# Kernel optimization log

Measured on AMD Instinct MI355X. Metric: run time of the kernel, lower is better.

## Reference

```python
import jax, jax.numpy as jnp
import numpy as np

N_NODES = 100000
N_EDGES = 1600000
NFEAT, NHID, NCLASS = 256, 512, 256


def _init_params(key):
    ks = jax.random.split(key, 8)
    s = 0.02
    p = {
        'W1a': jax.random.normal(ks[0], (NFEAT, NHID), jnp.float32) * s,
        'b1a': jnp.zeros((NHID,), jnp.float32),
        'W1b': jax.random.normal(ks[1], (NHID, NHID), jnp.float32) * s,
        'b1b': jnp.zeros((NHID,), jnp.float32),
        'W2a': jax.random.normal(ks[2], (NHID, NHID), jnp.float32) * s,
        'b2a': jnp.zeros((NHID,), jnp.float32),
        'W2b': jax.random.normal(ks[3], (NHID, NCLASS), jnp.float32) * s,
        'b2b': jnp.zeros((NCLASS,), jnp.float32),
        'eps1': jnp.zeros((), jnp.float32),
        'eps2': jnp.zeros((), jnp.float32),
    }
    return p


def setup_inputs() -> dict:
    key = jax.random.key(0)
    kx, ke, kp = jax.random.split(key, 3)
    x = jax.random.normal(kx, (N_NODES, NFEAT), jnp.float32)
    edge_index = jax.random.randint(ke, (2, N_EDGES), 0, N_NODES, jnp.int64)
    inp = {'x': x, 'edge_index': edge_index}
    inp.update(_init_params(kp))
    return inp


def _gin_agg(h, src, dst, eps, n_nodes):
    # sum of neighbor (source) features at each destination node + (1+eps)*self
    agg = jax.ops.segment_sum(h[src], dst, num_segments=n_nodes)
    return (1.0 + eps) * h + agg


def reference(x, edge_index, W1a, b1a, W1b, b1b, W2a, b2a, W2b, b2b, eps1, eps2):
    src, dst = edge_index[0], edge_index[1]
    n = x.shape[0]
    # GINConv layer 1: MLP = Linear-ReLU-Linear-ReLU
    h = _gin_agg(x, src, dst, eps1, n)
    h = jax.nn.relu(h @ W1a + b1a)
    h = jax.nn.relu(h @ W1b + b1b)
    # dropout: eval mode (identity)
    # GINConv layer 2: MLP = Linear-ReLU-Linear
    h = _gin_agg(h, src, dst, eps2, n)
    h = jax.nn.relu(h @ W2a + b2a)
    out = h @ W2b + b2b
    return out
```

## Files before the change

kernel.cpp:

```cpp
#include <hip/hip_runtime.h>
#include <hip/hip_bf16.h>
#include <stdint.h>

#define NN 100000
#define NFEATD 256
#define NHIDD 512
#define NCLASSD 256

typedef short bf16x8 __attribute__((ext_vector_type(8)));
typedef float f32x4 __attribute__((ext_vector_type(4)));
typedef float f32x2 __attribute__((ext_vector_type(2)));

__device__ __forceinline__ float bf2f(uint32_t u) {
    union { uint32_t i; float f; } v; v.i = u << 16; return v.f;
}
__device__ __forceinline__ ushort f2bf(float f) {
    uint32_t x = __float_as_uint(f);
    uint32_t r = (x + 0x7FFF + ((x >> 16) & 1)) >> 16;
    return (ushort)r;
}

__global__ void zero_i32(int* __restrict__ p, int n) {
    int i = blockIdx.x * 256 + threadIdx.x;
    if (i < n) p[i] = 0;
}

__global__ void count_deg(const int* __restrict__ dst, int* __restrict__ deg, int nE) {
    int e = blockIdx.x * 256 + threadIdx.x;
    if (e < nE) atomicAdd(&deg[dst[e]], 1);
}

__global__ __launch_bounds__(1024) void scan_excl(const int* __restrict__ deg,
                                                  int* __restrict__ off, int n) {
    __shared__ int wsum[16];
    __shared__ int carry_s;
    const int tid = threadIdx.x;
    const int lane = tid & 63, wv = tid >> 6;
    if (tid == 0) carry_s = 0;
    __syncthreads();
    for (int base = 0; base < n; base += 1024) {
        int i = base + tid;
        int v = (i < n) ? deg[i] : 0;
        int x = v;
#pragma unroll
        for (int d = 1; d < 64; d <<= 1) {
            int y = __shfl_up(x, d, 64);
            if (lane >= d) x += y;
        }
        if (lane == 63) wsum[wv] = x;
        __syncthreads();
        if (wv == 0 && lane < 16) {
            int s = wsum[lane];
#pragma unroll
            for (int d = 1; d < 16; d <<= 1) {
                int y = __shfl_up(s, d, 16);
                if (lane >= d) s += y;
            }
            wsum[lane] = s;
        }
        __syncthreads();
        int carry = carry_s;
        int wprefix = (wv == 0) ? 0 : wsum[wv - 1];
        if (i < n) off[i] = carry + wprefix + x - v;
        __syncthreads();
        if (tid == 0) carry_s = carry + wsum[15];
        __syncthreads();
    }
    if (tid == 0) off[n] = carry_s;
}

__global__ void fill_csr(const int* __restrict__ src, const int* __restrict__ dst,
                         const int* __restrict__ off, int* __restrict__ cursor,
                         int* __restrict__ csr, int nE) {
    int e = blockIdx.x * 256 + threadIdx.x;
    if (e >= nE) return;
    int d = dst[e];
    int p = off[d] + atomicAdd(&cursor[d], 1);
    csr[p] = src[e];
}

__global__ void prep_w4(const float* __restrict__ W1a, const float* __restrict__ W1b,
                        const float* __restrict__ W2a, const float* __restrict__ W2b,
                        ushort* __restrict__ Wt1a, ushort* __restrict__ Wt1b,
                        ushort* __restrict__ Wt2a, ushort* __restrict__ Wt2b) {
    int idx = blockIdx.x * 256 + threadIdx.x;
    if (idx < 131072) {
        int k = idx >> 9, n = idx & 511;
        Wt1a[n * 256 + k] = f2bf(W1a[idx]);
    } else if (idx < 131072 + 262144) {
        int i = idx - 131072;
        int k = i >> 9, n = i & 511;
        Wt1b[n * 512 + k] = f2bf(W1b[i]);
    } else if (idx < 131072 + 524288) {
        int i = idx - (131072 + 262144);
        int k = i >> 9, n = i & 511;
        Wt2a[n * 512 + k] = f2bf(W2a[i]);
    } else if (idx < 131072 + 524288 + 131072) {
        int i = idx - (131072 + 524288);
        int k = i >> 8, n = i & 255;
        Wt2b[n * 512 + k] = f2bf(W2b[i]);
    }
}

__global__ void cast_f32_fp8(const float* __restrict__ a, uint8_t* __restrict__ o, int n) {
    int i = (blockIdx.x * 256 + threadIdx.x) * 8;
    if (i >= n) return;
    float4 v0 = *(const float4*)(a + i);
    float4 v1 = *(const float4*)(a + i + 4);
    int lo = __builtin_amdgcn_cvt_pk_fp8_f32(v0.x, v0.y, 0, false);
    lo = __builtin_amdgcn_cvt_pk_fp8_f32(v0.z, v0.w, lo, true);
    int hi = __builtin_amdgcn_cvt_pk_fp8_f32(v1.x, v1.y, 0, false);
    hi = __builtin_amdgcn_cvt_pk_fp8_f32(v1.z, v1.w, hi, true);
    uint2 r; r.x = (uint32_t)lo; r.y = (uint32_t)hi;
    *(uint2*)(o + i) = r;
}

__device__ __forceinline__ void accp(uint32_t p, f32x2& lo, f32x2& hi) {
    lo += __builtin_amdgcn_cvt_pk_f32_fp8((int)p, false);
    hi += __builtin_amdgcn_cvt_pk_f32_fp8((int)p, true);
}

__global__ void gather256f8(const uint8_t* __restrict__ X8, const int* __restrict__ off,
                            const int* __restrict__ csr, const float* __restrict__ eps,
                            ushort* __restrict__ out) {
    int node = (blockIdx.x * 256 + threadIdx.x) >> 6;
    if (node >= NN) return;
    int lane = threadIdx.x & 63;
    float sc = 1.0f + *eps;
    f32x2 scv = {sc, sc};
    const uint32_t* X1 = (const uint32_t*)X8;
    f32x2 lo = {0.f, 0.f}, hi = {0.f, 0.f};
    {
        uint32_t p = X1[(size_t)node * 64 + lane];
        lo = scv * __builtin_amdgcn_cvt_pk_f32_fp8((int)p, false);
        hi = scv * __builtin_amdgcn_cvt_pk_f32_fp8((int)p, true);
    }
    int e = off[node], e1 = off[node + 1];
    for (; e + 7 < e1; e += 8) {
        uint32_t p[8];
#pragma unroll
        for (int t = 0; t < 8; ++t) p[t] = X1[(size_t)csr[e + t] * 64 + lane];
#pragma unroll
        for (int t = 0; t < 8; ++t) accp(p[t], lo, hi);
    }
    for (; e < e1; ++e)
        accp(X1[(size_t)csr[e] * 64 + lane], lo, hi);
    uint2 r;
    r.x = (uint32_t)f2bf(lo[0]) | ((uint32_t)f2bf(lo[1]) << 16);
    r.y = (uint32_t)f2bf(hi[0]) | ((uint32_t)f2bf(hi[1]) << 16);
    *(uint2*)(out + (size_t)node * 256 + lane * 4) = r;
}

__global__ void gather512f8(const uint8_t* __restrict__ H8, const int* __restrict__ off,
                            const int* __restrict__ csr, const float* __restrict__ eps,
                            ushort* __restrict__ out) {
    int node = (blockIdx.x * 256 + threadIdx.x) >> 6;
    if (node >= NN) return;
    int lane = threadIdx.x & 63;
    float sc = 1.0f + *eps;
    f32x2 scv = {sc, sc};
    const uint2* H2 = (const uint2*)H8;
    f32x2 l0 = {0.f, 0.f}, h0 = {0.f, 0.f}, l1 = {0.f, 0.f}, h1 = {0.f, 0.f};
    {
        uint2 p = H2[(size_t)node * 64 + lane];
        l0 = scv * __builtin_amdgcn_cvt_pk_f32_fp8((int)p.x, false);
        h0 = scv * __builtin_amdgcn_cvt_pk_f32_fp8((int)p.x, true);
        l1 = scv * __builtin_amdgcn_cvt_pk_f32_fp8((int)p.y, false);
        h1 = scv * __builtin_amdgcn_cvt_pk_f32_fp8((int)p.y, true);
    }
    int e = off[node], e1 = off[node + 1];
    for (; e + 7 < e1; e += 8) {
        uint2 p[8];
#pragma unroll
        for (int t = 0; t < 8; ++t) p[t] = H2[(size_t)csr[e + t] * 64 + lane];
#pragma unroll
        for (int t = 0; t < 8; ++t) {
            accp(p[t].x, l0, h0);
            accp(p[t].y, l1, h1);
        }
    }
    for (; e < e1; ++e) {
        uint2 p = H2[(size_t)csr[e] * 64 + lane];
        accp(p.x, l0, h0);
        accp(p.y, l1, h1);
    }
    uint4 r;
    r.x = (uint32_t)f2bf(l0[0]) | ((uint32_t)f2bf(l0[1]) << 16);
    r.y = (uint32_t)f2bf(h0[0]) | ((uint32_t)f2bf(h0[1]) << 16);
    r.z = (uint32_t)f2bf(l1[0]) | ((uint32_t)f2bf(l1[1]) << 16);
    r.w = (uint32_t)f2bf(h1[0]) | ((uint32_t)f2bf(h1[1]) << 16);
    *(uint4*)(out + (size_t)node * 512 + lane * 8) = r;
}


__device__ __forceinline__ void stage_a(const ushort* __restrict__ A, int K, int row0,
                                        int kc, ushort* dst, int tid, int Mm1) {
    int r = tid >> 2, c = tid & 3;
    int gr = row0 + r; if (gr > Mm1) gr = Mm1;
    const ushort* gp = A + (size_t)gr * K + kc + c * 8;
    __builtin_amdgcn_global_load_lds((const __attribute__((address_space(1))) void*)gp,
        (__attribute__((address_space(3))) void*)(dst + tid * 8), 16, 0, 0);
}

__device__ __forceinline__ void stage_b(const ushort* __restrict__ Bt, int K, int col0,
                                        int kc, ushort* dst, int tid) {
#pragma unroll
    for (int i = 0; i < 2; ++i) {
        int u = i * 512 + tid;
        int r = u >> 2, c = u & 3;
        const ushort* gp = Bt + (size_t)(col0 + r) * K + kc + c * 8;
        __builtin_amdgcn_global_load_lds((const __attribute__((address_space(1))) void*)gp,
            (__attribute__((address_space(3))) void*)(dst + u * 8), 16, 0, 0);
    }
}

__global__ __launch_bounds__(512, 4) void gemm_bt(
    const ushort* __restrict__ A, const ushort* __restrict__ Bt,
    const float* __restrict__ bias, float* __restrict__ outf,
    uint8_t* __restrict__ out8, ushort* __restrict__ outb,
    int M, int N, int K, int relu)
{
    __shared__ ushort smem[2][12288];
    const int tid = threadIdx.x;
    const int wave = tid >> 6, lane = tid & 63;
    const int quad = lane >> 4, lrow = lane & 15;
    const int wr = wave >> 2, wcn = wave & 3;
    const int nwg = gridDim.x;
    const int q = nwg >> 3, r8 = nwg & 7;
    const int xcd = blockIdx.x & 7, seq = blockIdx.x >> 3;
    const int k = ((xcd < r8) ? xcd * (q + 1) : r8 * (q + 1) + (xcd - r8) * q) + seq;
    const int ncol = N >> 8;
    const int row0 = (k / ncol) * 128, col0 = (k % ncol) * 256;
    const int NC = K >> 5;

    f32x4 acc[4][4] = {};

    stage_a(A, K, row0, 0, smem[0], tid, M - 1);
    stage_b(Bt, K, col0, 0, smem[0] + 4096, tid);
    __syncthreads();

    for (int t = 0; t < NC; ++t) {
        const ushort* As = smem[t & 1];
        const ushort* Bs = As + 4096;
        if (t + 1 < NC) {
            stage_a(A, K, row0, (t + 1) << 5, smem[(t + 1) & 1], tid, M - 1);
            stage_b(Bt, K, col0, (t + 1) << 5, smem[(t + 1) & 1] + 4096, tid);
        }
        bf16x8 af[4], bfr[4];
#pragma unroll
        for (int m = 0; m < 4; ++m)
            af[m] = *(const bf16x8*)(As + (wr * 64 + m * 16 + lrow) * 32 + quad * 8);
#pragma unroll
        for (int n = 0; n < 4; ++n)
            bfr[n] = *(const bf16x8*)(Bs + (wcn * 64 + n * 16 + lrow) * 32 + quad * 8);
        __builtin_amdgcn_s_setprio(1);
#pragma unroll
        for (int m = 0; m < 4; ++m)
#pragma unroll
            for (int n = 0; n < 4; ++n)
                acc[m][n] = __builtin_amdgcn_mfma_f32_16x16x32_bf16(bfr[n], af[m], acc[m][n], 0, 0, 0);
        __builtin_amdgcn_s_setprio(0);
        __syncthreads();
    }

#pragma unroll
    for (int m = 0; m < 4; ++m) {
        int rr = row0 + wr * 64 + m * 16 + lrow;
        if (rr < M) {
#pragma unroll
            for (int n = 0; n < 4; ++n) {
                int c = col0 + wcn * 64 + n * 16 + quad * 4;
                float4 bv = *(const float4*)(bias + c);
                float v0 = acc[m][n][0] + bv.x;
                float v1 = acc[m][n][1] + bv.y;
                float v2 = acc[m][n][2] + bv.z;
                float v3 = acc[m][n][3] + bv.w;
                if (relu) {
                    v0 = fmaxf(v0, 0.f); v1 = fmaxf(v1, 0.f);
                    v2 = fmaxf(v2, 0.f); v3 = fmaxf(v3, 0.f);
                }
                if (outf) {
                    float4 o; o.x = v0; o.y = v1; o.z = v2; o.w = v3;
                    *(float4*)(outf + (size_t)rr * N + c) = o;
                } else if (out8) {
                    int enc = __builtin_amdgcn_cvt_pk_fp8_f32(v0, v1, 0, false);
                    enc = __builtin_amdgcn_cvt_pk_fp8_f32(v2, v3, enc, true);
                    *(uint32_t*)(out8 + (size_t)rr * N + c) = (uint32_t)enc;
                } else {
                    uint2 o;
                    o.x = (uint32_t)f2bf(v0) | ((uint32_t)f2bf(v1) << 16);
                    o.y = (uint32_t)f2bf(v2) | ((uint32_t)f2bf(v3) << 16);
                    *(uint2*)(outb + (size_t)rr * N + c) = o;
                }
            }
        }
    }
}

extern "C" void kernel_launch(void* const* d_in, const int* in_sizes, int n_in,
                              void* d_out, int out_size, void* d_ws, size_t ws_size,
                              hipStream_t stream) {
    const float* x    = (const float*)d_in[0];
    const int*   ei   = (const int*)d_in[1];
    const float* W1a  = (const float*)d_in[2];
    const float* b1a  = (const float*)d_in[3];
    const float* W1b  = (const float*)d_in[4];
    const float* b1b  = (const float*)d_in[5];
    const float* W2a  = (const float*)d_in[6];
    const float* b2a  = (const float*)d_in[7];
    const float* W2b  = (const float*)d_in[8];
    const float* b2b  = (const float*)d_in[9];
    const float* eps1 = (const float*)d_in[10];
    const float* eps2 = (const float*)d_in[11];
    const int nE = in_sizes[1] / 2;
    const int* srcv = ei;
    const int* dstv = ei + nE;

    char* ws = (char*)d_ws;
    int*    off    = (int*)(ws);
    int*    cursor = (int*)(ws + 524288);
    int*    csr    = (int*)(ws + 1048576);
    ushort* Wt1a   = (ushort*)(ws + 8388608);
    ushort* Wt1b   = Wt1a + 512 * 256;
    ushort* Wt2a   = Wt1b + 512 * 512;
    ushort* Wt2b   = Wt2a + 512 * 512;
    char*   P      = ws + 10485760;
    char*   Q      = ws + 10485760 + 102400000;
    uint8_t* x8    = (uint8_t*)P;
    ushort* agg1b  = (ushort*)Q;
    ushort* h1     = (ushort*)P;
    uint8_t* h2f8  = (uint8_t*)Q;
    ushort* agg2b  = (ushort*)P;
    ushort* h3     = (ushort*)Q;

    zero_i32<<<(NN + 255) / 256, 256, 0, stream>>>(cursor, NN);
    count_deg<<<(nE + 255) / 256, 256, 0, stream>>>(dstv, cursor, nE);
    scan_excl<<<1, 1024, 0, stream>>>(cursor, off, NN);
    zero_i32<<<(NN + 255) / 256, 256, 0, stream>>>(cursor, NN);
    fill_csr<<<(nE + 255) / 256, 256, 0, stream>>>(srcv, dstv, off, cursor, csr, nE);

    prep_w4<<<(786432 + 255) / 256, 256, 0, stream>>>(W1a, W1b, W2a, W2b,
                                                      Wt1a, Wt1b, Wt2a, Wt2b);
    cast_f32_fp8<<<(NN * NFEATD / 8 + 255) / 256, 256, 0, stream>>>(x, x8, NN * NFEATD);

    gather256f8<<<(NN * 64) / 256, 256, 0, stream>>>(x8, off, csr, eps1, agg1b);
    const int nrow = (NN + 127) / 128;
    gemm_bt<<<nrow * (NHIDD / 256), 512, 0, stream>>>(agg1b, Wt1a, b1a, nullptr, nullptr, h1, NN, NHIDD, NFEATD, 1);
    gemm_bt<<<nrow * (NHIDD / 256), 512, 0, stream>>>(h1, Wt1b, b1b, nullptr, h2f8, nullptr, NN, NHIDD, NHIDD, 1);

    gather512f8<<<(NN * 64) / 256, 256, 0, stream>>>(h2f8, off, csr, eps2, agg2b);
    gemm_bt<<<nrow * (NHIDD / 256), 512, 0, stream>>>(agg2b, Wt2a, b2a, nullptr, nullptr, h3, NN, NHIDD, NHIDD, 1);
    gemm_bt<<<nrow * (NCLASSD / 256), 512, 0, stream>>>(h3, Wt2b, b2b, (float*)d_out, nullptr, nullptr, NN, NCLASSD, NHIDD, 0);
}
```

Baseline: 925.2 us.

## Fuse CSR preprocessing kernels and parallelize the degree prefix scan

Result: faster. 837.8 us (-9.4%).

```diff
diff --git a/kernel.cpp b/kernel.cpp
--- a/kernel.cpp
+++ b/kernel.cpp
@@ -25,94 +25,112 @@
     if (i < n) p[i] = 0;
 }
 
-__global__ void count_deg(const int* __restrict__ dst, int* __restrict__ deg, int nE) {
-    int e = blockIdx.x * 256 + threadIdx.x;
-    if (e < nE) atomicAdd(&deg[dst[e]], 1);
-}
-
-__global__ __launch_bounds__(1024) void scan_excl(const int* __restrict__ deg,
-                                                  int* __restrict__ off, int n) {
-    __shared__ int wsum[16];
-    __shared__ int carry_s;
-    const int tid = threadIdx.x;
-    const int lane = tid & 63, wv = tid >> 6;
-    if (tid == 0) carry_s = 0;
+__global__ void fused_misc(const int* __restrict__ dst, int* __restrict__ deg, int nE, int cb,
+                           const float* __restrict__ W1a, const float* __restrict__ W1b,
+                           const float* __restrict__ W2a, const float* __restrict__ W2b,
+                           ushort* __restrict__ Wt1a, ushort* __restrict__ Wt1b,
+                           ushort* __restrict__ Wt2a, ushort* __restrict__ Wt2b,
+                           const float* __restrict__ x, uint8_t* __restrict__ x8, int nx) {
+    int b = blockIdx.x;
+    if (b < cb) {
+        int e = b * 256 + threadIdx.x;
+        if (e < nE) atomicAdd(&deg[dst[e]], 1);
+    } else if (b < cb + 3072) {
+        int idx = (b - cb) * 256 + threadIdx.x;
+        if (idx < 131072) {
+            int k = idx >> 9, n = idx & 511;
+            Wt1a[n * 256 + k] = f2bf(W1a[idx]);
+        } else if (idx < 131072 + 262144) {
+            int i = idx - 131072;
+            int k = i >> 9, n = i & 511;
+            Wt1b[n * 512 + k] = f2bf(W1b[i]);
+        } else if (idx < 131072 + 524288) {
+            int i = idx - (131072 + 262144);
+            int k = i >> 9, n = i & 511;
+            Wt2a[n * 512 + k] = f2bf(W2a[i]);
+        } else {
+            int i = idx - (131072 + 524288);
+            int k = i >> 8, n = i & 255;
+            Wt2b[n * 512 + k] = f2bf(W2b[i]);
+        }
+    } else {
+        int i = ((b - cb - 3072) * 256 + threadIdx.x) * 8;
+        if (i < nx) {
+            float4 v0 = *(const float4*)(x + i);
+            float4 v1 = *(const float4*)(x + i + 4);
+            int lo = __builtin_amdgcn_cvt_pk_fp8_f32(v0.x, v0.y, 0, false);
+            lo = __builtin_amdgcn_cvt_pk_fp8_f32(v0.z, v0.w, lo, true);
+            int hi = __builtin_amdgcn_cvt_pk_fp8_f32(v1.x, v1.y, 0, false);
+            hi = __builtin_amdgcn_cvt_pk_fp8_f32(v1.z, v1.w, hi, true);
+            uint2 r; r.x = (uint32_t)lo; r.y = (uint32_t)hi;
+            *(uint2*)(x8 + i) = r;
+        }
+    }
+}
+
+__global__ void scan_part(const int* __restrict__ deg, int* __restrict__ part, int n) {
+    int base = blockIdx.x * 512;
+    int tid = threadIdx.x;
+    int i0 = base + tid * 2;
+    int v0 = (i0 < n) ? deg[i0] : 0;
+    int v1 = (i0 + 1 < n) ? deg[i0 + 1] : 0;
+    int s = v0 + v1;
+#pragma unroll
+    for (int d = 1; d < 64; d <<= 1) s += __shfl_xor(s, d, 64);
+    __shared__ int ws[4];
+    if ((tid & 63) == 0) ws[tid >> 6] = s;
     __syncthreads();
-    for (int base = 0; base < n; base += 1024) {
-        int i = base + tid;
-        int v = (i < n) ? deg[i] : 0;
-        int x = v;
-#pragma unroll
-        for (int d = 1; d < 64; d <<= 1) {
-            int y = __shfl_up(x, d, 64);
-            if (lane >= d) x += y;
-        }
-        if (lane == 63) wsum[wv] = x;
-        __syncthreads();
-        if (wv == 0 && lane < 16) {
-            int s = wsum[lane];
-#pragma unroll
-            for (int d = 1; d < 16; d <<= 1) {
-                int y = __shfl_up(s, d, 16);
-                if (lane >= d) s += y;
-            }
-            wsum[lane] = s;
-        }
-        __syncthreads();
-        int carry = carry_s;
-        int wprefix = (wv == 0) ? 0 : wsum[wv - 1];
-        if (i < n) off[i] = carry + wprefix + x - v;
-        __syncthreads();
-        if (tid == 0) carry_s = carry + wsum[15];
-        __syncthreads();
-    }
-    if (tid == 0) off[n] = carry_s;
-}
-
-__global__ void fill_csr(const int* __restrict__ src, const int* __restrict__ dst,
-                         const int* __restrict__ off, int* __restrict__ cursor,
-                         int* __restrict__ csr, int nE) {
+    if (tid == 0) part[blockIdx.x] = ws[0] + ws[1] + ws[2] + ws[3];
+}
+
+__global__ void scan_mid(int* __restrict__ part, int* __restrict__ total, int np) {
+    int tid = threadIdx.x;
+    int lane = tid & 63, wv = tid >> 6;
+    int v = (tid < np) ? part[tid] : 0;
+    int x = v;
+#pragma unroll
+    for (int d = 1; d < 64; d <<= 1) { int y = __shfl_up(x, d, 64); if (lane >= d) x += y; }
+    __shared__ int ws[4];
+    if (lane == 63) ws[wv] = x;
+    __syncthreads();
+    int wp = 0;
+#pragma unroll
+    for (int j = 0; j < 4; ++j) if (j < wv) wp += ws[j];
+    if (tid < np) part[tid] = wp + x - v;
+    if (tid == 255) total[0] = wp + x;
+}
+
+__global__ void scan_apply(const int* __restrict__ deg, const int* __restrict__ part,
+                           int* __restrict__ off, int n) {
+    int base = blockIdx.x * 512;
+    int tid = threadIdx.x;
+    int lane = tid & 63, wv = tid >> 6;
+    int i0 = base + tid * 2;
+    int v0 = (i0 < n) ? deg[i0] : 0;
+    int v1 = (i0 + 1 < n) ? deg[i0 + 1] : 0;
+    int s = v0 + v1;
+    int x = s;
+#pragma unroll
+    for (int d = 1; d < 64; d <<= 1) { int y = __shfl_up(x, d, 64); if (lane >= d) x += y; }
+    __shared__ int ws[4];
+    if (lane == 63) ws[wv] = x;
+    __syncthreads();
+    int wp = 0;
+#pragma unroll
+    for (int j = 0; j < 4; ++j) if (j < wv) wp += ws[j];
+    int excl = part[blockIdx.x] + wp + x - s;
+    if (i0 < n) off[i0] = excl;
+    if (i0 + 1 < n) off[i0 + 1] = excl + v0;
+}
+
+__global__ void fill_csr2(const int* __restrict__ src, const int* __restrict__ dst,
+                          const int* __restrict__ off, int* __restrict__ deg,
+                          int* __restrict__ csr, int nE) {
     int e = blockIdx.x * 256 + threadIdx.x;
     if (e >= nE) return;
     int d = dst[e];
-    int p = off[d] + atomicAdd(&cursor[d], 1);
-    csr[p] = src[e];
-}
-
-__global__ void prep_w4(const float* __restrict__ W1a, const float* __restrict__ W1b,
-                        const float* __restrict__ W2a, const float* __restrict__ W2b,
-                        ushort* __restrict__ Wt1a, ushort* __restrict__ Wt1b,
-                        ushort* __restrict__ Wt2a, ushort* __restrict__ Wt2b) {
-    int idx = blockIdx.x * 256 + threadIdx.x;
-    if (idx < 131072) {
-        int k = idx >> 9, n = idx & 511;
-        Wt1a[n * 256 + k] = f2bf(W1a[idx]);
-    } else if (idx < 131072 + 262144) {
-        int i = idx - 131072;
-        int k = i >> 9, n = i & 511;
-        Wt1b[n * 512 + k] = f2bf(W1b[i]);
-    } else if (idx < 131072 + 524288) {
-        int i = idx - (131072 + 262144);
-        int k = i >> 9, n = i & 511;
-        Wt2a[n * 512 + k] = f2bf(W2a[i]);
-    } else if (idx < 131072 + 524288 + 131072) {
-        int i = idx - (131072 + 524288);
-        int k = i >> 8, n = i & 255;
-        Wt2b[n * 512 + k] = f2bf(W2b[i]);
-    }
-}
-
-__global__ void cast_f32_fp8(const float* __restrict__ a, uint8_t* __restrict__ o, int n) {
-    int i = (blockIdx.x * 256 + threadIdx.x) * 8;
-    if (i >= n) return;
-    float4 v0 = *(const float4*)(a + i);
-    float4 v1 = *(const float4*)(a + i + 4);
-    int lo = __builtin_amdgcn_cvt_pk_fp8_f32(v0.x, v0.y, 0, false);
-    lo = __builtin_amdgcn_cvt_pk_fp8_f32(v0.z, v0.w, lo, true);
-    int hi = __builtin_amdgcn_cvt_pk_fp8_f32(v1.x, v1.y, 0, false);
-    hi = __builtin_amdgcn_cvt_pk_fp8_f32(v1.z, v1.w, hi, true);
-    uint2 r; r.x = (uint32_t)lo; r.y = (uint32_t)hi;
-    *(uint2*)(o + i) = r;
+    int r = atomicSub(&deg[d], 1);
+    csr[off[d] + r - 1] = src[e];
 }
 
 __device__ __forceinline__ void accp(uint32_t p, f32x2& lo, f32x2& hi) {
@@ -318,7 +336,8 @@
 
     char* ws = (char*)d_ws;
     int*    off    = (int*)(ws);
-    int*    cursor = (int*)(ws + 524288);
+    int*    part   = (int*)(ws + 458752);
+    int*    deg    = (int*)(ws + 524288);
     int*    csr    = (int*)(ws + 1048576);
     ushort* Wt1a   = (ushort*)(ws + 8388608);
     ushort* Wt1b   = Wt1a + 512 * 256;
@@ -333,15 +352,18 @@
     ushort* agg2b  = (ushort*)P;
     ushort* h3     = (ushort*)Q;
 
-    zero_i32<<<(NN + 255) / 256, 256, 0, stream>>>(cursor, NN);
-    count_deg<<<(nE + 255) / 256, 256, 0, stream>>>(dstv, cursor, nE);
-    scan_excl<<<1, 1024, 0, stream>>>(cursor, off, NN);
-    zero_i32<<<(NN + 255) / 256, 256, 0, stream>>>(cursor, NN);
-    fill_csr<<<(nE + 255) / 256, 256, 0, stream>>>(srcv, dstv, off, cursor, csr, nE);
-
-    prep_w4<<<(786432 + 255) / 256, 256, 0, stream>>>(W1a, W1b, W2a, W2b,
-                                                      Wt1a, Wt1b, Wt2a, Wt2b);
-    cast_f32_fp8<<<(NN * NFEATD / 8 + 255) / 256, 256, 0, stream>>>(x, x8, NN * NFEATD);
+    const int cb = (nE + 255) / 256;
+    const int castb = (NN * NFEATD / 8 + 255) / 256;
+    zero_i32<<<(NN + 255) / 256, 256, 0, stream>>>(deg, NN);
+    fused_misc<<<cb + 3072 + castb, 256, 0, stream>>>(dstv, deg, nE, cb,
+                                                      W1a, W1b, W2a, W2b,
+                                                      Wt1a, Wt1b, Wt2a, Wt2b,
+                                                      x, x8, NN * NFEATD);
+    const int nsb = (NN + 511) / 512;
+    scan_part<<<nsb, 256, 0, stream>>>(deg, part, NN);
+    scan_mid<<<1, 256, 0, stream>>>(part, off + NN, nsb);
+    scan_apply<<<nsb, 256, 0, stream>>>(deg, part, off, NN);
+    fill_csr2<<<cb, 256, 0, stream>>>(srcv, dstv, off, deg, csr, nE);
 
     gather256f8<<<(NN * 64) / 256, 256, 0, stream>>>(x8, off, csr, eps1, agg1b);
     const int nrow = (NN + 127) / 128;
```
